# Optimization experiments

Hardware: AMD Instinct MI355X
Metric: run time of the kernel (lower is better)

The kernel has to match this reference:

```python
import jax, jax.numpy as jnp
import numpy as np

B, T, D, H = 32, 2048, 1024, 128


def setup_inputs() -> dict:
    key = jax.random.key(0)
    ks = jax.random.split(key, 7)
    s = 1.0 / np.sqrt(D)
    return {
        "x": jax.random.normal(ks[0], (B, T, D), dtype=jnp.float32),
        "Wk": jax.random.normal(ks[1], (D, H), dtype=jnp.float32) * s,
        "bk": jax.random.normal(ks[2], (H,), dtype=jnp.float32) * 0.01,
        "Wq": jax.random.normal(ks[3], (D, H), dtype=jnp.float32) * s,
        "bq": jax.random.normal(ks[4], (H,), dtype=jnp.float32) * 0.01,
        "Wv": jax.random.normal(ks[5], (D, H), dtype=jnp.float32) * s,
        "bv": jax.random.normal(ks[6], (H,), dtype=jnp.float32) * 0.01,
    }


def reference(x, Wk, bk, Wq, bq, Wv, bv):
    # Single causal attention head. NOTE faithful quirk: scores = K @ Q^T.
    k = x @ Wk + bk  # [B,T,H]
    q = x @ Wq + bq  # [B,T,H]
    v = x @ Wv + bv  # [B,T,H]
    scale = k.shape[-1] ** -0.5
    wei = jnp.einsum("bth,bsh->bts", k, q) * scale  # [B,T,T], K on the left
    t = x.shape[1]
    causal = jnp.tril(jnp.ones((t, t), dtype=bool))
    wei = jnp.where(causal, wei, -jnp.inf)
    wei = jax.nn.softmax(wei, axis=-1)
    # dropout is eval-mode identity (deterministic reference)
    out = jnp.einsum("bts,bsh->bth", wei, v)  # [B,T,H]
    return out
```

## Files before the change

### kernel.cpp

```cpp
#include <hip/hip_runtime.h>
#include <hip/hip_bf16.h>
#include <stdint.h>

typedef __bf16 bf16;
typedef __bf16 bf16x8 __attribute__((ext_vector_type(8)));
typedef __bf16 bf16x4 __attribute__((ext_vector_type(4)));
typedef float f32x4 __attribute__((ext_vector_type(4)));
typedef float f32x8 __attribute__((ext_vector_type(8)));

#define BB 32
#define TT 2048
#define DD 1024
#define HH 128
#define SCALE 0.08838834764831845f
#define LOG2E 1.4426950408889634f
#define KS (SCALE * LOG2E)

__device__ __forceinline__ void gl_lds16(const bf16* g, bf16* l) {
  __builtin_amdgcn_global_load_lds((__attribute__((address_space(1))) const void*)g,
                                   (__attribute__((address_space(3))) void*)l,
                                   16, 0, 0);
}
__device__ __forceinline__ void gl_lds16f(const float* g, float* l) {
  __builtin_amdgcn_global_load_lds((__attribute__((address_space(1))) const void*)g,
                                   (__attribute__((address_space(3))) void*)l,
                                   16, 0, 0);
}

__global__ __launch_bounds__(256) void prep_w(const float* __restrict__ Wk,
                                              const float* __restrict__ Wq,
                                              const float* __restrict__ Wv,
                                              const float* __restrict__ bk,
                                              const float* __restrict__ bq,
                                              const float* __restrict__ bv,
                                              bf16* __restrict__ Wt,
                                              float* __restrict__ bcat) {
  int tid = blockIdx.x * 256 + threadIdx.x;
  if (tid < 384) {
    int mat = tid >> 7, h = tid & 127;
    float bb = (mat == 0) ? bk[h] : (mat == 1) ? bq[h] : bv[h];
    bcat[tid] = (mat == 0) ? bb * KS : bb;
  }
  int mat = tid >> 14;
  int r = tid & 16383;
  int h = r & 127;
  int d0 = (r >> 7) << 3;
  const float* W = (mat == 0) ? Wk : (mat == 1) ? Wq : Wv;
  const float ks = (mat == 0) ? KS : 1.0f;
  bf16x8 v;
#pragma unroll
  for (int i = 0; i < 8; ++i) v[i] = (bf16)(W[(size_t)(d0 + i) * HH + h] * ks);
  *(bf16x8*)(Wt + ((size_t)mat * HH + h) * DD + d0) = v;
}

__global__ __launch_bounds__(256, 2) void qkv_proj(
    const float* __restrict__ x, const bf16* __restrict__ Wt,
    const float* __restrict__ bcat,
    bf16* __restrict__ kb, bf16* __restrict__ qb, bf16* __restrict__ Vt) {
  const int bid = blockIdx.x;
  const int tid = threadIdx.x;
  const int lane = tid & 63;
  const int w = tid >> 6;
  const int l15 = lane & 15, l4 = lane >> 4;
  const size_t row0 = (size_t)bid * 64;
  const int colbase = w * 96;

  __shared__ __attribute__((aligned(16))) float As[2][64][32];
  __shared__ __attribute__((aligned(16))) bf16  Ws[2][384][32];

  f32x4 acc[4][6];
#pragma unroll
  for (int m = 0; m < 4; ++m)
#pragma unroll
    for (int n = 0; n < 6; ++n) acc[m][n] = f32x4{0.f, 0.f, 0.f, 0.f};

  auto stage = [&](int buf, int k0) {
#pragma unroll
    for (int i = 0; i < 2; ++i) {
      int base = i * 256 + w * 64;
      int L = base + lane;
      int r = L >> 3, c = L & 7;
      const float* src = x + (row0 + r) * DD + k0 + ((c ^ (r & 7)) << 2);
      gl_lds16f(src, &As[buf][0][0] + (size_t)base * 4);
    }
#pragma unroll
    for (int i = 0; i < 6; ++i) {
      int base = i * 256 + w * 64;
      int L = base + lane;
      int col = L >> 2, j = L & 3;
      const bf16* src = Wt + (size_t)col * DD + k0 + ((j ^ ((col >> 1) & 3)) << 3);
      gl_lds16(src, &Ws[buf][0][0] + (size_t)base * 8);
    }
  };

  stage(0, 0);
  __syncthreads();

  for (int step = 0; step < 32; ++step) {
    const int cur = step & 1;
    if (step + 1 < 32) stage(cur ^ 1, (step + 1) * 32);

    bf16x8 af[4];
#pragma unroll
    for (int m = 0; m < 4; ++m) {
      int r = m * 16 + l15;
      int c0 = (2 * l4) ^ (r & 7), c1 = (2 * l4 + 1) ^ (r & 7);
      f32x4 lo = *(const f32x4*)&As[cur][r][c0 * 4];
      f32x4 hi = *(const f32x4*)&As[cur][r][c1 * 4];
#pragma unroll
      for (int i = 0; i < 4; ++i) { af[m][i] = (bf16)lo[i]; af[m][4 + i] = (bf16)hi[i]; }
    }
    bf16x8 bfr[6];
#pragma unroll
    for (int n = 0; n < 6; ++n) {
      int col = colbase + n * 16 + l15;
      bfr[n] = *(const bf16x8*)&Ws[cur][col][(l4 ^ ((col >> 1) & 3)) * 8];
    }
#pragma unroll
    for (int m = 0; m < 4; ++m)
#pragma unroll
      for (int n = 0; n < 6; ++n)
        acc[m][n] = __builtin_amdgcn_mfma_f32_16x16x32_bf16(af[m], bfr[n],
                                                            acc[m][n], 0, 0, 0);
    __syncthreads();
  }

  float bvv[6];
#pragma unroll
  for (int n = 0; n < 6; ++n) bvv[n] = bcat[colbase + n * 16 + l15];

  const int bidx = bid >> 5;
  const int tloc0 = (bid & 31) * 64;
#pragma unroll
  for (int m = 0; m < 4; ++m)
#pragma unroll
    for (int n = 0; n < 6; ++n) {
      int col = colbase + n * 16 + l15;
      int mat = col >> 7;
      int hcol = col & 127;
      if (mat == 2) {
        bf16x4 v4;
#pragma unroll
        for (int e = 0; e < 4; ++e) v4[e] = (bf16)(acc[m][n][e] + bvv[n]);
        int t = tloc0 + m * 16 + l4 * 4;
        *(bf16x4*)(Vt + ((size_t)bidx * HH + hcol) * TT + t) = v4;
      } else {
        bf16* dst = (mat == 0) ? kb : qb;
#pragma unroll
        for (int e = 0; e < 4; ++e) {
          size_t rowg = row0 + m * 16 + l4 * 4 + e;
          dst[rowg * HH + hcol] = (bf16)(acc[m][n][e] + bvv[n]);
        }
      }
    }
}

__global__ __launch_bounds__(256, 3) void attn(const bf16* __restrict__ kb,
                                               const bf16* __restrict__ qb,
                                               const bf16* __restrict__ Vt,
                                               float* __restrict__ out) {
  const int bid = blockIdx.x;
  const int b = bid & 31;
  const int p = bid >> 5;
  const int tid = threadIdx.x;
  const int lane = tid & 63;
  const int w = tid >> 6;
  const int l15 = lane & 15, l4 = lane >> 4;

  __shared__ __attribute__((aligned(16))) bf16 Es[64 * 128];
  __shared__ __attribute__((aligned(16))) bf16 Vs[128 * 64];
  __shared__ __attribute__((aligned(16))) bf16 Ps[4][16 * 72];

  for (int job = 0; job < 2; ++job) {
    const int tile = job ? p : (31 - p);
    const int t0 = tile * 64;

    bf16x8 af[4];
    {
      const bf16* kp = kb + ((size_t)b * TT + t0 + w * 16 + l15) * HH + l4 * 8;
#pragma unroll
      for (int kc = 0; kc < 4; ++kc) af[kc] = *(const bf16x8*)(kp + kc * 32);
    }

    f32x4 o[8];
#pragma unroll
    for (int j = 0; j < 8; ++j) o[j] = f32x4{0.f, 0.f, 0.f, 0.f};
    float mrow[4], lrow[4];
#pragma unroll
    for (int e = 0; e < 4; ++e) { mrow[e] = -1e30f; lrow[e] = 0.f; }

    const int nst = tile + 1;
    for (int jt = 0; jt < nst; ++jt) {
      const int s0 = jt * 64;
      {
        const bf16* Eg = qb + ((size_t)b * TT + s0) * HH;
#pragma unroll
        for (int it = 0; it < 4; ++it) {
          int L = w * 256 + it * 64 + lane;
          int er = L >> 4, ec = L & 15;
          int ecs = ec ^ (er & 7);
          gl_lds16(Eg + er * HH + ecs * 8, Es + (size_t)(w * 256 + it * 64) * 8);
        }
        const bf16* Vg = Vt + (size_t)b * HH * TT + s0;
#pragma unroll
        for (int it = 0; it < 4; ++it) {
          int L = w * 256 + it * 64 + lane;
          int vr = L >> 3, vc = L & 7;
          int vcs = vc ^ (vr & 7);
          gl_lds16(Vg + (size_t)vr * TT + vcs * 8, Vs + (size_t)(w * 256 + it * 64) * 8);
        }
      }
      __syncthreads();

      f32x4 s[4];
#pragma unroll
      for (int j = 0; j < 4; ++j) s[j] = f32x4{0.f, 0.f, 0.f, 0.f};
#pragma unroll
      for (int kc = 0; kc < 4; ++kc) {
        bf16x8 ef[4];
#pragma unroll
        for (int fn = 0; fn < 4; ++fn) {
          int er = fn * 16 + l15;
          int c = kc * 4 + l4;
          int cs = c ^ (er & 7);
          ef[fn] = *(const bf16x8*)&Es[er * 128 + cs * 8];
        }
#pragma unroll
        for (int fn = 0; fn < 4; ++fn)
          s[fn] = __builtin_amdgcn_mfma_f32_16x16x32_bf16(af[kc], ef[fn],
                                                          s[fn], 0, 0, 0);
      }

      if (s0 + 63 > t0 + w * 16) {
#pragma unroll
        for (int fn = 0; fn < 4; ++fn)
#pragma unroll
          for (int e = 0; e < 4; ++e) {
            int tg = t0 + w * 16 + l4 * 4 + e;
            int sg = s0 + fn * 16 + l15;
            if (sg > tg) s[fn][e] = -1e30f;
          }
      }

      float mx[4];
#pragma unroll
      for (int e = 0; e < 4; ++e) {
        float m = fmaxf(fmaxf(s[0][e], s[1][e]), fmaxf(s[2][e], s[3][e]));
#pragma unroll
        for (int d = 1; d < 16; d <<= 1) m = fmaxf(m, __shfl_xor(m, d));
        mx[e] = m;
      }
      float g = fmaxf(fmaxf(mx[0] - mrow[0], mx[1] - mrow[1]),
                      fmaxf(mx[2] - mrow[2], mx[3] - mrow[3]));
      if (!__all(g <= 8.0f)) {
#pragma unroll
        for (int e = 0; e < 4; ++e) {
          float mn = fmaxf(mrow[e], mx[e]);
          float rsc = exp2f(mrow[e] - mn);
          lrow[e] *= rsc;
#pragma unroll
          for (int fh = 0; fh < 8; ++fh) o[fh][e] *= rsc;
          mrow[e] = mn;
        }
      }
#pragma unroll
      for (int e = 0; e < 4; ++e) {
        float ps = 0.f;
#pragma unroll
        for (int fn = 0; fn < 4; ++fn) {
          float pv = exp2f(s[fn][e] - mrow[e]);
          s[fn][e] = pv;
          ps += pv;
        }
#pragma unroll
        for (int d = 1; d < 16; d <<= 1) ps += __shfl_xor(ps, d);
        lrow[e] += ps;
      }

#pragma unroll
      for (int fn = 0; fn < 4; ++fn)
#pragma unroll
        for (int e = 0; e < 4; ++e)
          Ps[w][(l4 * 4 + e) * 72 + fn * 16 + l15] = (bf16)s[fn][e];

#pragma unroll
      for (int kc = 0; kc < 2; ++kc) {
        bf16x8 pf = *(const bf16x8*)&Ps[w][l15 * 72 + kc * 32 + l4 * 8];
#pragma unroll
        for (int fh = 0; fh < 8; ++fh) {
          int vr = fh * 16 + l15;
          int c = kc * 4 + l4;
          int cs = c ^ (vr & 7);
          bf16x8 vf = *(const bf16x8*)&Vs[vr * 64 + cs * 8];
          o[fh] = __builtin_amdgcn_mfma_f32_16x16x32_bf16(pf, vf, o[fh], 0, 0, 0);
        }
      }
      __syncthreads();
    }

#pragma unroll
    for (int e = 0; e < 4; ++e) {
      float rl = 1.0f / lrow[e];
      int tg = t0 + w * 16 + l4 * 4 + e;
#pragma unroll
      for (int fh = 0; fh < 8; ++fh)
        out[((size_t)b * TT + tg) * HH + fh * 16 + l15] = o[fh][e] * rl;
    }
  }
}

extern "C" void kernel_launch(void* const* d_in, const int* in_sizes, int n_in,
                              void* d_out, int out_size, void* d_ws, size_t ws_size,
                              hipStream_t stream) {
  (void)in_sizes; (void)n_in; (void)out_size; (void)ws_size;
  const float* x  = (const float*)d_in[0];
  const float* Wk = (const float*)d_in[1];
  const float* bk = (const float*)d_in[2];
  const float* Wq = (const float*)d_in[3];
  const float* bq = (const float*)d_in[4];
  const float* Wv = (const float*)d_in[5];
  const float* bv = (const float*)d_in[6];
  float* out = (float*)d_out;

  const size_t NTH = (size_t)BB * TT * HH;
  bf16* kb = (bf16*)d_ws;
  bf16* qb = kb + NTH;
  bf16* Vt = qb + NTH;
  bf16* Wt = Vt + NTH;
  float* bcat = (float*)(Wt + (size_t)3 * HH * DD);

  prep_w<<<192, 256, 0, stream>>>(Wk, Wq, Wv, bk, bq, bv, Wt, bcat);
  qkv_proj<<<1024, 256, 0, stream>>>(x, Wt, bcat, kb, qb, Vt);
  attn<<<512, 256, 0, stream>>>(kb, qb, Vt, out);
}
```

Baseline: 213.8 us.

## Enlarge QKV projection tile to 128 rows with 8 waves per block

The QKV projection block grows from 64 to 128 rows of x, using 512 threads arranged as 2 row-groups by 4 column-groups. Each block still loads the full 384-column weight slice, so weight LDS traffic per row is halved and the block count drops from 1024 to 512. The cost is a doubled x LDS buffer, fewer blocks to spread across CUs, and more LDS use per block, which could lower occupancy.

```diff
diff --git a/kernel.cpp b/kernel.cpp
--- a/kernel.cpp
+++ b/kernel.cpp
@@ -53,7 +53,7 @@
   *(bf16x8*)(Wt + ((size_t)mat * HH + h) * DD + d0) = v;
 }
 
-__global__ __launch_bounds__(256, 2) void qkv_proj(
+__global__ __launch_bounds__(512, 2) void qkv_proj(
     const float* __restrict__ x, const bf16* __restrict__ Wt,
     const float* __restrict__ bcat,
     bf16* __restrict__ kb, bf16* __restrict__ qb, bf16* __restrict__ Vt) {
@@ -61,12 +61,14 @@
   const int tid = threadIdx.x;
   const int lane = tid & 63;
   const int w = tid >> 6;
+  const int wr = w >> 2, wc = w & 3;
   const int l15 = lane & 15, l4 = lane >> 4;
-  const size_t row0 = (size_t)bid * 64;
-  const int colbase = w * 96;
-
-  __shared__ __attribute__((aligned(16))) float As[2][64][32];
-  __shared__ __attribute__((aligned(16))) bf16  Ws[2][384][32];
+  const size_t row0 = (size_t)bid * 128;
+  const int colbase = wc * 96;
+  const int rowbase = wr * 64;
+
+  __shared__ __attribute__((aligned(16))) float As[2][128 * 32];
+  __shared__ __attribute__((aligned(16))) bf16  Ws[2][384 * 32];
 
   f32x4 acc[4][6];
 #pragma unroll
@@ -77,19 +79,19 @@
   auto stage = [&](int buf, int k0) {
 #pragma unroll
     for (int i = 0; i < 2; ++i) {
-      int base = i * 256 + w * 64;
-      int L = base + lane;
-      int r = L >> 3, c = L & 7;
+      int base = i * 512 + (w << 6);
+      int C = base + lane;
+      int r = C >> 3, c = C & 7;
       const float* src = x + (row0 + r) * DD + k0 + ((c ^ (r & 7)) << 2);
-      gl_lds16f(src, &As[buf][0][0] + (size_t)base * 4);
-    }
-#pragma unroll
-    for (int i = 0; i < 6; ++i) {
-      int base = i * 256 + w * 64;
-      int L = base + lane;
-      int col = L >> 2, j = L & 3;
+      gl_lds16f(src, &As[buf][0] + (size_t)base * 4);
+    }
+#pragma unroll
+    for (int i = 0; i < 3; ++i) {
+      int base = i * 512 + (w << 6);
+      int C = base + lane;
+      int col = C >> 2, j = C & 3;
       const bf16* src = Wt + (size_t)col * DD + k0 + ((j ^ ((col >> 1) & 3)) << 3);
-      gl_lds16(src, &Ws[buf][0][0] + (size_t)base * 8);
+      gl_lds16(src, &Ws[buf][0] + (size_t)base * 8);
     }
   };
 
@@ -100,27 +102,27 @@
     const int cur = step & 1;
     if (step + 1 < 32) stage(cur ^ 1, (step + 1) * 32);
 
-    bf16x8 af[4];
+    bf16x8 afm[4];
 #pragma unroll
     for (int m = 0; m < 4; ++m) {
-      int r = m * 16 + l15;
+      int r = rowbase + m * 16 + l15;
       int c0 = (2 * l4) ^ (r & 7), c1 = (2 * l4 + 1) ^ (r & 7);
-      f32x4 lo = *(const f32x4*)&As[cur][r][c0 * 4];
-      f32x4 hi = *(const f32x4*)&As[cur][r][c1 * 4];
-#pragma unroll
-      for (int i = 0; i < 4; ++i) { af[m][i] = (bf16)lo[i]; af[m][4 + i] = (bf16)hi[i]; }
+      f32x4 lo = *(const f32x4*)&As[cur][r * 32 + c0 * 4];
+      f32x4 hi = *(const f32x4*)&As[cur][r * 32 + c1 * 4];
+#pragma unroll
+      for (int i = 0; i < 4; ++i) { afm[m][i] = (bf16)lo[i]; afm[m][4 + i] = (bf16)hi[i]; }
     }
     bf16x8 bfr[6];
 #pragma unroll
     for (int n = 0; n < 6; ++n) {
       int col = colbase + n * 16 + l15;
-      bfr[n] = *(const bf16x8*)&Ws[cur][col][(l4 ^ ((col >> 1) & 3)) * 8];
+      bfr[n] = *(const bf16x8*)&Ws[cur][col * 32 + ((l4 ^ ((col >> 1) & 3)) << 3)];
     }
 #pragma unroll
     for (int m = 0; m < 4; ++m)
 #pragma unroll
       for (int n = 0; n < 6; ++n)
-        acc[m][n] = __builtin_amdgcn_mfma_f32_16x16x32_bf16(af[m], bfr[n],
+        acc[m][n] = __builtin_amdgcn_mfma_f32_16x16x32_bf16(afm[m], bfr[n],
                                                             acc[m][n], 0, 0, 0);
     __syncthreads();
   }
@@ -129,8 +131,8 @@
 #pragma unroll
   for (int n = 0; n < 6; ++n) bvv[n] = bcat[colbase + n * 16 + l15];
 
-  const int bidx = bid >> 5;
-  const int tloc0 = (bid & 31) * 64;
+  const int bidx = bid >> 4;
+  const int tloc0 = (bid & 15) * 128;
 #pragma unroll
   for (int m = 0; m < 4; ++m)
 #pragma unroll
@@ -138,19 +140,17 @@
       int col = colbase + n * 16 + l15;
       int mat = col >> 7;
       int hcol = col & 127;
+      int rloc = rowbase + m * 16 + l4 * 4;
       if (mat == 2) {
         bf16x4 v4;
 #pragma unroll
         for (int e = 0; e < 4; ++e) v4[e] = (bf16)(acc[m][n][e] + bvv[n]);
-        int t = tloc0 + m * 16 + l4 * 4;
-        *(bf16x4*)(Vt + ((size_t)bidx * HH + hcol) * TT + t) = v4;
+        *(bf16x4*)(Vt + ((size_t)bidx * HH + hcol) * TT + tloc0 + rloc) = v4;
       } else {
         bf16* dst = (mat == 0) ? kb : qb;
 #pragma unroll
-        for (int e = 0; e < 4; ++e) {
-          size_t rowg = row0 + m * 16 + l4 * 4 + e;
-          dst[rowg * HH + hcol] = (bf16)(acc[m][n][e] + bvv[n]);
-        }
+        for (int e = 0; e < 4; ++e)
+          dst[(row0 + rloc + e) * HH + hcol] = (bf16)(acc[m][n][e] + bvv[n]);
       }
     }
 }
@@ -330,6 +330,6 @@
   float* bcat = (float*)(Wt + (size_t)3 * HH * DD);
 
   prep_w<<<192, 256, 0, stream>>>(Wk, Wq, Wv, bk, bq, bv, Wt, bcat);
-  qkv_proj<<<1024, 256, 0, stream>>>(x, Wt, bcat, kb, qb, Vt);
+  qkv_proj<<<512, 512, 0, stream>>>(x, Wt, bcat, kb, qb, Vt);
   attn<<<512, 256, 0, stream>>>(kb, qb, Vt, out);
 }
```

Measured after the change: 212.8 us. No clear change (-0.5%).
